# Performance work log

Hardware: AMD Instinct MI355X
Metric: run time of the kernel (lower is better)

## Reference

```python
import jax, jax.numpy as jnp
import numpy as np

N, D, H, L, T, R = 50000, 128, 8, 2, 4, 8
E = 800000
HD = D // H  # head_size = 16
SQRT_D = float(np.sqrt(HD))


def typed_linear(x, types, W):
    # x: (n, Din), types: (n,), W: (T, Din, Dout)  -- per-type dense projection
    out = jnp.zeros((x.shape[0], W.shape[-1]), x.dtype)
    for t in range(W.shape[0]):
        out = out + jnp.where((types == t)[:, None], x @ W[t], 0.0)
    return out


def rel_typed(x, etype, W):
    # x: (E, H, d), etype: (E,), W: (H, R, d, d) -- per-head, per-edge-type linear
    out = jnp.zeros_like(x)
    for r in range(W.shape[1]):
        out = out + jnp.where((etype == r)[:, None, None], jnp.einsum('ehd,hdo->eho', x, W[:, r]), 0.0)
    return out


def edge_softmax(a, dst, n):
    # softmax over incoming edges per destination node, per head. a: (E, H)
    amax = jax.ops.segment_max(a, dst, num_segments=n)
    amax = jnp.where(jnp.isfinite(amax), amax, 0.0)
    ex = jnp.exp(a - amax[dst])
    s = jax.ops.segment_sum(ex, dst, num_segments=n)
    return ex / (s[dst] + 1e-9)


def layer_norm(x, g, b, eps=1e-5):
    mu = x.mean(-1, keepdims=True)
    var = ((x - mu) ** 2).mean(-1, keepdims=True)
    return (x - mu) * jax.lax.rsqrt(var + eps) * g + b


def hgt_conv(x, ntype, etype, src, dst, Wk, Wq, Wv, Wa, ratt, rmsg, rpri, skip):
    n = x.shape[0]
    k = typed_linear(x, ntype, Wk).reshape(n, H, HD)
    q = typed_linear(x, ntype, Wq).reshape(n, H, HD)
    v = typed_linear(x, ntype, Wv).reshape(n, H, HD)
    kw = rel_typed(k[src], etype, ratt)               # (E, H, d)
    pri = rpri[:, etype].T                            # (E, H)
    a = (kw * q[dst]).sum(-1) * pri / SQRT_D          # (E, H)
    m = rel_typed(v[src], etype, rmsg)                # (E, H, d)
    att = edge_softmax(a, dst, n)                     # (E, H)
    h = jax.ops.segment_sum(m * att[..., None], dst, num_segments=n)
    h = h.reshape(n, D)
    h = typed_linear(h, ntype, Wa)                    # dropout off (eval)
    alpha = jax.nn.sigmoid(skip[ntype])[:, None]
    return h * alpha + x * (1.0 - alpha)


def setup_inputs() -> dict:
    key = jax.random.key(0)
    ks = jax.random.split(key, 12)
    g_lin = float(np.sqrt(2.0 / (D + D)))   # xavier-ish scale for D x D
    g_rel = float(np.sqrt(2.0 / (HD + HD)))
    g_emb = float(np.sqrt(2.0 / (N + D)))
    return {
        'embed': jax.random.normal(ks[0], (T, N, D), jnp.float32) * g_emb,
        'Wk': jax.random.normal(ks[1], (L, T, D, D), jnp.float32) * g_lin,
        'Wq': jax.random.normal(ks[2], (L, T, D, D), jnp.float32) * g_lin,
        'Wv': jax.random.normal(ks[3], (L, T, D, D), jnp.float32) * g_lin,
        'Wa': jax.random.normal(ks[4], (L, T, D, D), jnp.float32) * g_lin,
        'rel_att': jax.random.normal(ks[5], (L, H, R, HD, HD), jnp.float32) * g_rel,
        'rel_msg': jax.random.normal(ks[6], (L, H, R, HD, HD), jnp.float32) * g_rel,
        'rel_pri': jnp.ones((L, H, R), jnp.float32),
        'skip': jnp.ones((L, T), jnp.float32),
        'ln_g': jnp.ones((L, D), jnp.float32),
        'ln_b': jnp.zeros((L, D), jnp.float32),
        'src': jax.random.randint(ks[7], (E,), 0, N, jnp.int32),
        'dst': jax.random.randint(ks[8], (E,), 0, N, jnp.int32),
        'ntype': jax.random.randint(ks[9], (N,), 0, T, jnp.int32),
        'etype': jax.random.randint(ks[10], (E,), 0, R, jnp.int32),
    }


def reference(embed, Wk, Wq, Wv, Wa, rel_att, rel_msg, rel_pri, skip, ln_g, ln_b, src, dst, ntype, etype):
    # masked per-type embedding init: node gets row <rank-within-its-type> of its type table
    onehot = jax.nn.one_hot(ntype, T, dtype=jnp.int32)
    rank = jnp.take_along_axis(jnp.cumsum(onehot, axis=0), ntype[:, None], axis=1)[:, 0] - 1
    h = embed[ntype, rank]                            # (N, D)
    for l in range(L):
        h_prev = h
        hc = hgt_conv(h, ntype, etype, src, dst,
                      Wk[l], Wq[l], Wv[l], Wa[l],
                      rel_att[l], rel_msg[l], rel_pri[l], skip[l])
        h = layer_norm(hc, ln_g[l], ln_b[l]) + h_prev
    return h
```

## Files before the change

kernel.cpp:

```cpp
#include <hip/hip_runtime.h>
#include <math.h>

#define N_NODES 50000
#define DIM     128
#define NHEAD   8
#define HDIM    16
#define NLAYER  2
#define NTYPE   4
#define NREL    8
#define NEDGE   800000
#define RB      256
#define GN      8
#define MT      32
#define NK      (N_NODES * NREL)
#define LHR     (NLAYER * NHEAD * NREL)

typedef __attribute__((ext_vector_type(8))) short bf16x8;
typedef __attribute__((ext_vector_type(4))) float f32x4;

__device__ __forceinline__ float blo(unsigned w) { return __uint_as_float(w << 16); }
__device__ __forceinline__ float bhi(unsigned w) { return __uint_as_float(w & 0xFFFF0000u); }
__device__ __forceinline__ unsigned short f2bf(float f) {
    unsigned b = __float_as_uint(f);
    b += 0x7FFFu + ((b >> 16) & 1u);
    return (unsigned short)(b >> 16);
}
__device__ __forceinline__ bf16x8 pack8(float4 x0, float4 x1) {
    bf16x8 r;
    r[0] = (short)f2bf(x0.x); r[1] = (short)f2bf(x0.y);
    r[2] = (short)f2bf(x0.z); r[3] = (short)f2bf(x0.w);
    r[4] = (short)f2bf(x1.x); r[5] = (short)f2bf(x1.y);
    r[6] = (short)f2bf(x1.z); r[7] = (short)f2bf(x1.w);
    return r;
}
__device__ __forceinline__ bf16x8 zero8() {
    bf16x8 r;
    #pragma unroll
    for (int j = 0; j < 8; j++) r[j] = 0;
    return r;
}


__global__ void k_hist(const int* __restrict__ ntype, int* __restrict__ hist, int n) {
    __shared__ int cnt[NTYPE];
    if (threadIdx.x < NTYPE) cnt[threadIdx.x] = 0;
    __syncthreads();
    int i = blockIdx.x * RB + threadIdx.x;
    if (i < n) atomicAdd(&cnt[ntype[i]], 1);
    __syncthreads();
    if (threadIdx.x < NTYPE) hist[blockIdx.x * NTYPE + threadIdx.x] = cnt[threadIdx.x];
}

__global__ void k_prefix(const int* __restrict__ hist, int* __restrict__ off, int nb) {
    int t = threadIdx.x;
    if (t >= NTYPE) return;
    int acc = 0;
    for (int b = 0; b < nb; b++) { off[b * NTYPE + t] = acc; acc += hist[b * NTYPE + t]; }
}

__global__ void k_rank(const int* __restrict__ ntype, const int* __restrict__ off,
                       int* __restrict__ rank, int n) {
    __shared__ int ty[RB];
    int i = blockIdx.x * RB + threadIdx.x;
    int t = (i < n) ? ntype[i] : -1;
    ty[threadIdx.x] = t;
    __syncthreads();
    if (i < n) {
        int c = 0;
        for (int j = 0; j < (int)threadIdx.x; j++) c += (ty[j] == t);
        rank[i] = off[blockIdx.x * NTYPE + t] + c;
    }
}

__global__ void k_embed(const float* __restrict__ embed, const int* __restrict__ ntype,
                        const int* __restrict__ rank, float* __restrict__ h) {
    int i = blockIdx.x;
    int t = ntype[i], r = rank[i];
    h[(size_t)i * DIM + threadIdx.x] = embed[((size_t)t * N_NODES + r) * DIM + threadIdx.x];
}

__global__ void k_typeoff(const int* __restrict__ hist, const int* __restrict__ boff,
                          int nb, int* __restrict__ typeoff) {
    if (threadIdx.x == 0 && blockIdx.x == 0) {
        int acc = 0;
        for (int t = 0; t < NTYPE; t++) {
            typeoff[t] = acc;
            acc += boff[(nb - 1) * NTYPE + t] + hist[(nb - 1) * NTYPE + t];
        }
    }
}

__global__ void k_perm(const int* __restrict__ ntype, const int* __restrict__ rank,
                       const int* __restrict__ typeoff, int* __restrict__ perm,
                       int* __restrict__ iperm, int n) {
    int i = blockIdx.x * 256 + threadIdx.x;
    if (i < n) {
        int p = typeoff[ntype[i]] + rank[i];
        perm[p] = i;
        iperm[i] = p;
    }
}


__global__ void k_deg2(const int* __restrict__ dst, const int* __restrict__ etype,
                       int* __restrict__ deg) {
    int e = blockIdx.x * 256 + threadIdx.x;
    if (e < NEDGE) atomicAdd(&deg[dst[e] * NREL + etype[e]], 1);
}

__global__ void k_scan1(const int* __restrict__ deg, int* __restrict__ rs,
                        int* __restrict__ bsum, int n) {
    __shared__ int sh[256];
    int i = blockIdx.x * 256 + threadIdx.x;
    int v = (i < n) ? deg[i] : 0;
    sh[threadIdx.x] = v;
    __syncthreads();
    for (int off = 1; off < 256; off <<= 1) {
        int x = (threadIdx.x >= off) ? sh[threadIdx.x - off] : 0;
        __syncthreads();
        sh[threadIdx.x] += x;
        __syncthreads();
    }
    if (i < n) rs[i] = sh[threadIdx.x] - v;
    if (threadIdx.x == 255) bsum[blockIdx.x] = sh[255];
}

__global__ void k_scan2b(int* __restrict__ bsum, int nb) {
    __shared__ int sh[256];
    __shared__ int carry;
    if (threadIdx.x == 0) carry = 0;
    __syncthreads();
    for (int base = 0; base < nb; base += 256) {
        int i = base + threadIdx.x;
        int v = (i < nb) ? bsum[i] : 0;
        sh[threadIdx.x] = v;
        __syncthreads();
        for (int off = 1; off < 256; off <<= 1) {
            int x = (threadIdx.x >= off) ? sh[threadIdx.x - off] : 0;
            __syncthreads();
            sh[threadIdx.x] += x;
            __syncthreads();
        }
        if (i < nb) bsum[i] = sh[threadIdx.x] - v + carry;
        __syncthreads();
        if (threadIdx.x == 0) carry += sh[255];
        __syncthreads();
    }
}

__global__ void k_scan3(int* __restrict__ rs, const int* __restrict__ bsum, int n) {
    int i = blockIdx.x * 256 + threadIdx.x;
    if (i < n) rs[i] += bsum[blockIdx.x];
    if (i == 0) rs[n] = NEDGE;
}

__global__ void k_scatter2(const int* __restrict__ src, const int* __restrict__ dst,
                           const int* __restrict__ etype, const int* __restrict__ iperm,
                           const int* __restrict__ rs,
                           int* __restrict__ cur, int* __restrict__ epk) {
    int e = blockIdx.x * 256 + threadIdx.x;
    if (e < NEDGE) {
        int et = etype[e];
        int key = dst[e] * NREL + et;
        int p = atomicAdd(&cur[key], 1);
        epk[rs[key] + p] = iperm[src[e]] | (et << 24);
    }
}


__global__ void k_rattB(const float* __restrict__ ratt, unsigned short* __restrict__ rattB) {
    int i = blockIdx.x * 256 + threadIdx.x;
    rattB[i] = f2bf(ratt[i]);
}

__global__ void k_rmsgT(const float* __restrict__ rmsg, float* __restrict__ rmsgT) {
    int b = blockIdx.x;
    int d = threadIdx.x >> 4, o = threadIdx.x & 15;
    rmsgT[b * 256 + o * 16 + d] = rmsg[b * 256 + d * 16 + o];
}

__global__ void k_rmsgBP(const float* __restrict__ rmsg, unsigned short* __restrict__ out) {
    int b = blockIdx.x;
    int i = threadIdx.x;
    int ln = i >> 3, e = i & 7;
    int half = ln >> 4;
    unsigned short v = 0;
    if (half < 2) v = f2bf(rmsg[(size_t)b * 256 + (half * 8 + e) * 16 + (ln & 15)]);
    out[(size_t)b * 512 + i] = v;
}

__global__ void k_rattBP(const float* __restrict__ ratt, const float* __restrict__ rpri,
                         unsigned short* __restrict__ out) {
    int b = blockIdx.x;
    int i = threadIdx.x;
    int ln = i >> 3, e = i & 7;
    int half = ln >> 4;
    int et = b % NREL;
    int hh = (b / NREL) % NHEAD;
    int l = b / (NREL * NHEAD);
    float scale = rpri[(l * NHEAD + hh) * NREL + et] * 0.25f;
    unsigned short v = 0;
    if (half < 2) v = f2bf(ratt[(size_t)b * 256 + (half * 8 + e) * 16 + (ln & 15)] * scale);
    out[(size_t)b * 512 + i] = v;
}

__global__ void k_packW_all(const float* __restrict__ Wk, const float* __restrict__ Wq,
                            const float* __restrict__ Wv, unsigned short* __restrict__ wpk) {
    int bid = blockIdx.x;
    int t = bid & 3;
    int m = (bid >> 2) % 3;
    int l = bid / 12;
    const float* W = (m == 0 ? Wk : (m == 1 ? Wq : Wv)) + ((size_t)l * NTYPE + t) * 16384;
    unsigned short* ob = wpk + (size_t)bid * 16384;
    for (int idx = threadIdx.x; idx < 16384; idx += 256) {
        int ct = idx >> 11, kc = (idx >> 9) & 3, ln = (idx >> 3) & 63, j = idx & 7;
        int k = kc * 32 + ((ln >> 4) << 3) + j;
        int c = ct * 16 + (ln & 15);
        ob[idx] = f2bf(W[k * 128 + c]);
    }
}


template<int FULL>
__global__ __launch_bounds__(256) void k_qkv_mfma(
        const float* __restrict__ h, const int* __restrict__ perm, const int* __restrict__ ntype,
        const float* __restrict__ Wk, const float* __restrict__ Wq, const float* __restrict__ Wv,
        const unsigned short* __restrict__ WkB, const unsigned short* __restrict__ WqB,
        const unsigned short* __restrict__ WvB,
        const unsigned short* __restrict__ rattBP, const unsigned short* __restrict__ rmsgBP,
        const float* __restrict__ rmsgT,
        unsigned short* __restrict__ kb, float* __restrict__ qout,
        unsigned short* __restrict__ vt, unsigned short* __restrict__ tab, int n) {
    int tid = threadIdx.x;
    int base = blockIdx.x * MT;
    __shared__ int nodes_s[MT];
    __shared__ int types_s[MT];
    __shared__ unsigned short vs[MT][136];
    __shared__ unsigned short ks[MT][136];

    if (tid < MT) {
        int idx = base + tid;
        int nd = (idx < n) ? perm[idx] : -1;
        nodes_s[tid] = nd;
        types_s[tid] = (nd >= 0) ? ntype[nd] : -1;
    }
    __syncthreads();
    bool same = (nodes_s[MT - 1] >= 0) && (types_s[0] == types_s[MT - 1]);
    int l = tid & 63, w = tid >> 6;

    if (same) {
        int t = types_s[0];
        const unsigned short* wbk = WkB + (size_t)t * 16384;
        const unsigned short* wbq = WqB + (size_t)t * 16384;
        const unsigned short* wbv = WvB + (size_t)t * 16384;
        f32x4 acc[3][2][2];
        #pragma unroll
        for (int m = 0; m < 3; m++)
            #pragma unroll
            for (int a = 0; a < 2; a++)
                #pragma unroll
                for (int b = 0; b < 2; b++) {
                    acc[m][a][b][0] = 0.f; acc[m][a][b][1] = 0.f;
                    acc[m][a][b][2] = 0.f; acc[m][a][b][3] = 0.f;
                }
        #pragma unroll 1
        for (int kc = 0; kc < 4; kc++) {
            int koff = kc * 32 + ((l >> 4) << 3);
            int r0 = l & 15;
            const float4* p0 = (const float4*)(h + (size_t)nodes_s[r0] * DIM + koff);
            bf16x8 a0 = pack8(p0[0], p0[1]);
            const float4* p1 = (const float4*)(h + (size_t)nodes_s[16 + r0] * DIM + koff);
            bf16x8 a1 = pack8(p1[0], p1[1]);
            #pragma unroll
            for (int cti = 0; cti < 2; cti++) {
                int boff = ((w * 2 + cti) * 4 + kc) * 512 + l * 8;
                bf16x8 bk = *(const bf16x8*)(wbk + boff);
                acc[0][0][cti] = __builtin_amdgcn_mfma_f32_16x16x32_bf16(a0, bk, acc[0][0][cti], 0, 0, 0);
                acc[0][1][cti] = __builtin_amdgcn_mfma_f32_16x16x32_bf16(a1, bk, acc[0][1][cti], 0, 0, 0);
                bf16x8 bq = *(const bf16x8*)(wbq + boff);
                acc[1][0][cti] = __builtin_amdgcn_mfma_f32_16x16x32_bf16(a0, bq, acc[1][0][cti], 0, 0, 0);
                acc[1][1][cti] = __builtin_amdgcn_mfma_f32_16x16x32_bf16(a1, bq, acc[1][1][cti], 0, 0, 0);
                bf16x8 bv = *(const bf16x8*)(wbv + boff);
                acc[2][0][cti] = __builtin_amdgcn_mfma_f32_16x16x32_bf16(a0, bv, acc[2][0][cti], 0, 0, 0);
                acc[2][1][cti] = __builtin_amdgcn_mfma_f32_16x16x32_bf16(a1, bv, acc[2][1][cti], 0, 0, 0);
            }
        }
        #pragma unroll
        for (int mt = 0; mt < 2; mt++)
            #pragma unroll
            for (int cti = 0; cti < 2; cti++) {
                int col = w * 32 + cti * 16 + (l & 15);
                #pragma unroll
                for (int r = 0; r < 4; r++) {
                    int row = mt * 16 + ((l >> 4) << 2) + r;
                    size_t p = (size_t)(base + row) * DIM + col;
                    qout[p] = acc[1][mt][cti][r];
                    vs[row][col] = f2bf(acc[2][mt][cti][r]);
                    unsigned short kv = f2bf(acc[0][mt][cti][r]);
                    ks[row][col] = kv;
                    if constexpr (!FULL) kb[p] = kv;
                }
            }
    } else {
        int o = tid & 127, half = tid >> 7;
        for (int nn = half; nn < MT; nn += 2) {
            int nd = nodes_s[nn];
            if (nd < 0) { vs[nn][o] = 0; ks[nn][o] = 0; continue; }
            int t = types_s[nn];
            const float* wk = Wk + (size_t)t * 16384;
            const float* wq = Wq + (size_t)t * 16384;
            const float* wv = Wv + (size_t)t * 16384;
            float ak = 0.f, aq = 0.f, av = 0.f;
            for (int d = 0; d < DIM; d++) {
                float xv = h[(size_t)nd * DIM + d];
                ak = fmaf(xv, wk[d * DIM + o], ak);
                aq = fmaf(xv, wq[d * DIM + o], aq);
                av = fmaf(xv, wv[d * DIM + o], av);
            }
            size_t p = (size_t)(base + nn) * DIM + o;
            qout[p] = aq;
            vs[nn][o] = f2bf(av);
            unsigned short kv = f2bf(ak);
            ks[nn][o] = kv;
            if constexpr (!FULL) kb[p] = kv;
        }
    }
    __syncthreads();

    if constexpr (FULL) {
        __shared__ unsigned short tab_s[MT][264];
        int half = l >> 4;
        bf16x8 afrk[2][2], afrv[2][2];
        #pragma unroll
        for (int hh2 = 0; hh2 < 2; hh2++) {
            int hh = w * 2 + hh2;
            #pragma unroll
            for (int nt = 0; nt < 2; nt++) {
                if (half < 2) {
                    afrk[hh2][nt] = *(const bf16x8*)&ks[nt * 16 + (l & 15)][hh * HDIM + half * 8];
                    afrv[hh2][nt] = *(const bf16x8*)&vs[nt * 16 + (l & 15)][hh * HDIM + half * 8];
                } else {
                    afrk[hh2][nt] = zero8();
                    afrv[hh2][nt] = zero8();
                }
            }
        }
        #pragma unroll 1
        for (int et = 0; et < NREL; et++) {
            #pragma unroll
            for (int hh2 = 0; hh2 < 2; hh2++) {
                int hh = w * 2 + hh2;
                bf16x8 bfa = *(const bf16x8*)(rattBP + ((size_t)(hh * NREL + et) * 64 + l) * 8);
                bf16x8 bfm = *(const bf16x8*)(rmsgBP + ((size_t)(hh * NREL + et) * 64 + l) * 8);
                #pragma unroll
                for (int nt = 0; nt < 2; nt++) {
                    f32x4 dk = {0.f, 0.f, 0.f, 0.f};
                    dk = __builtin_amdgcn_mfma_f32_16x16x32_bf16(afrk[hh2][nt], bfa, dk, 0, 0, 0);
                    f32x4 dv = {0.f, 0.f, 0.f, 0.f};
                    dv = __builtin_amdgcn_mfma_f32_16x16x32_bf16(afrv[hh2][nt], bfm, dv, 0, 0, 0);
                    #pragma unroll
                    for (int r = 0; r < 4; r++) {
                        int row = nt * 16 + half * 4 + r;
                        tab_s[row][hh * HDIM + (l & 15)] = f2bf(dk[r]);
                        tab_s[row][128 + hh * HDIM + (l & 15)] = f2bf(dv[r]);
                    }
                }
            }
            __syncthreads();
            #pragma unroll
            for (int it = 0; it < 4; it++) {
                int idx = it * 256 + tid;
                int row = idx >> 5;
                int c8 = idx & 31;
                if (base + row < n)
                    *(uint4*)&tab[((size_t)(base + row) * NREL + et) * 256 + c8 * 8] =
                        *(const uint4*)&tab_s[row][c8 * 8];
            }
            __syncthreads();
        }
    } else {
        int o = tid & 127, half = tid >> 7;
        int hh = o >> 4, oo = o & 15;
        #pragma unroll 1
        for (int et = 0; et < NREL; et++) {
            const float4* wm4 = (const float4*)(rmsgT + ((size_t)(hh * NREL + et) * HDIM + oo) * HDIM);
            float4 m0 = wm4[0], m1 = wm4[1], m2 = wm4[2], m3 = wm4[3];
            for (int i = 0; i < 16; i++) {
                int nn = half * 16 + i;
                if (base + nn >= n) continue;
                const uint4* vr = (const uint4*)&vs[nn][hh * HDIM];
                uint4 v0 = vr[0], v1 = vr[1];
                float vv = blo(v0.x)*m0.x + bhi(v0.x)*m0.y + blo(v0.y)*m0.z + bhi(v0.y)*m0.w
                         + blo(v0.z)*m1.x + bhi(v0.z)*m1.y + blo(v0.w)*m1.z + bhi(v0.w)*m1.w
                         + blo(v1.x)*m2.x + bhi(v1.x)*m2.y + blo(v1.y)*m2.z + bhi(v1.y)*m2.w
                         + blo(v1.z)*m3.x + bhi(v1.z)*m3.y + blo(v1.w)*m3.z + bhi(v1.w)*m3.w;
                vt[((size_t)(base + nn) * NREL + et) * DIM + o] = f2bf(vv);
            }
        }
    }
}


__global__ __launch_bounds__(128) void k_fused12(
        const unsigned short* __restrict__ tab, const float* __restrict__ qbuf,
        const int* __restrict__ perm,
        const int* __restrict__ rs2, const int* __restrict__ epk,
        float* __restrict__ agg) {
    int b = blockIdx.x;
    int node = perm[b];
    int tid = threadIdx.x;
    int hh = tid >> 4, oo = tid & 15;
    int wv = tid >> 6;
    int hl = hh & 3;

    __shared__ float q_s[DIM];
    __shared__ float a_sw[2][4][HDIM + 1];
    __shared__ int   es_sw[2][HDIM];

    int e0 = rs2[node * NREL];
    int e1 = rs2[node * NREL + NREL];
    if (e0 == e1) { agg[(size_t)b * DIM + tid] = 0.f; return; }

    q_s[tid] = qbuf[(size_t)b * DIM + tid];
    const float4* q4 = (const float4*)&q_s[hh * HDIM];
    float4 q0 = q4[0], q1 = q4[1], q2 = q4[2], q3 = q4[3];

    float m_h = -1e30f, s_h = 0.f, out = 0.f;

    for (int w0e = e0; w0e < e1; w0e += HDIM) {
        int cnt = min(HDIM, e1 - w0e);
        float a = -1e30f;
        int pk = 0;
        if (oo < cnt) {
            pk = epk[w0e + oo];
            int sv = pk & 0x00FFFFFF;
            int et = ((unsigned)pk) >> 24;
            const uint4* kw = (const uint4*)(tab + ((size_t)sv * NREL + et) * 256 + hh * HDIM);
            uint4 ka = kw[0], kc = kw[1];
            a = blo(ka.x)*q0.x + bhi(ka.x)*q0.y + blo(ka.y)*q0.z + bhi(ka.y)*q0.w
              + blo(ka.z)*q1.x + bhi(ka.z)*q1.y + blo(ka.w)*q1.z + bhi(ka.w)*q1.w
              + blo(kc.x)*q2.x + bhi(kc.x)*q2.y + blo(kc.y)*q2.z + bhi(kc.y)*q2.w
              + blo(kc.z)*q3.x + bhi(kc.z)*q3.y + blo(kc.w)*q3.z + bhi(kc.w)*q3.w;
        }
        if (hl == 0) es_sw[wv][oo] = pk;
        float cmax = a;
        cmax = fmaxf(cmax, __shfl_xor(cmax, 1));
        cmax = fmaxf(cmax, __shfl_xor(cmax, 2));
        cmax = fmaxf(cmax, __shfl_xor(cmax, 4));
        cmax = fmaxf(cmax, __shfl_xor(cmax, 8));
        float m_t = (cmax > m_h + 12.f) ? cmax : m_h;
        float r = __expf(m_h - m_t);
        s_h *= r; out *= r; m_h = m_t;
        float p = (oo < cnt) ? __expf(a - m_h) : 0.f;
        float ps = p;
        ps += __shfl_xor(ps, 1);
        ps += __shfl_xor(ps, 2);
        ps += __shfl_xor(ps, 4);
        ps += __shfl_xor(ps, 8);
        s_h += ps;
        a_sw[wv][hl][oo] = p;
        for (int c = 0; c < cnt; c++) {
            float pc = a_sw[wv][hl][c];
            int pkc = es_sw[wv][c];
            int sv = pkc & 0x00FFFFFF;
            int et = ((unsigned)pkc) >> 24;
            unsigned short uv = tab[((size_t)sv * NREL + et) * 256 + 128 + tid];
            out = fmaf(pc, __uint_as_float((unsigned)uv << 16), out);
        }
    }

    agg[(size_t)b * DIM + tid] = out / (s_h + 1e-9f);
}


__global__ __launch_bounds__(128) void k_fused11(
        const unsigned short* __restrict__ kb, const float* __restrict__ qbuf,
        const unsigned short* __restrict__ vt,
        const int* __restrict__ perm,
        const int* __restrict__ rs2, const int* __restrict__ epk,
        const unsigned short* __restrict__ rattB, const float* __restrict__ rpri,
        float* __restrict__ agg) {
    int b = blockIdx.x;
    int node = perm[b];
    int tid = threadIdx.x;
    int hh = tid >> 4, oo = tid & 15;
    int wv = tid >> 6;
    int hl = hh & 3;

    __shared__ float q_s[DIM];
    __shared__ float u_s[NREL][NHEAD * HDIM + 4];
    __shared__ float a_sw[2][4][HDIM + 1];
    __shared__ int   es_sw[2][HDIM];

    int e0 = rs2[node * NREL];
    int e1 = rs2[node * NREL + NREL];
    if (e0 == e1) { agg[(size_t)b * DIM + tid] = 0.f; return; }

    q_s[tid] = qbuf[(size_t)b * DIM + tid];
    {
        const float4* q4 = (const float4*)&q_s[hh * HDIM];
        float4 q0 = q4[0], q1 = q4[1], q2 = q4[2], q3 = q4[3];
        #pragma unroll
        for (int et = 0; et < NREL; et++) {
            const uint4* wB = (const uint4*)(rattB + ((size_t)(hh * NREL + et) * HDIM + oo) * HDIM);
            uint4 wa = wB[0], wb = wB[1];
            float s = blo(wa.x)*q0.x + bhi(wa.x)*q0.y + blo(wa.y)*q0.z + bhi(wa.y)*q0.w
                    + blo(wa.z)*q1.x + bhi(wa.z)*q1.y + blo(wa.w)*q1.z + bhi(wa.w)*q1.w
                    + blo(wb.x)*q2.x + bhi(wb.x)*q2.y + blo(wb.y)*q2.z + bhi(wb.y)*q2.w
                    + blo(wb.z)*q3.x + bhi(wb.z)*q3.y + blo(wb.w)*q3.z + bhi(wb.w)*q3.w;
            u_s[et][tid] = s * rpri[hh * NREL + et] * 0.25f;
        }
    }

    float m_h = -1e30f, s_h = 0.f, out = 0.f;

    for (int w0e = e0; w0e < e1; w0e += HDIM) {
        int cnt = min(HDIM, e1 - w0e);
        float a = -1e30f;
        int pk = 0;
        if (oo < cnt) {
            pk = epk[w0e + oo];
            int sv = pk & 0x00FFFFFF;
            int et = ((unsigned)pk) >> 24;
            const uint4* kr = (const uint4*)(kb + (size_t)sv * DIM + hh * HDIM);
            uint4 ka = kr[0], kc = kr[1];
            const float4* u4 = (const float4*)&u_s[et][hh * HDIM];
            float4 u0 = u4[0], u1 = u4[1], u2 = u4[2], u3 = u4[3];
            a = blo(ka.x)*u0.x + bhi(ka.x)*u0.y + blo(ka.y)*u0.z + bhi(ka.y)*u0.w
              + blo(ka.z)*u1.x + bhi(ka.z)*u1.y + blo(ka.w)*u1.z + bhi(ka.w)*u1.w
              + blo(kc.x)*u2.x + bhi(kc.x)*u2.y + blo(kc.y)*u2.z + bhi(kc.y)*u2.w
              + blo(kc.z)*u3.x + bhi(kc.z)*u3.y + blo(kc.w)*u3.z + bhi(kc.w)*u3.w;
        }
        if (hl == 0) es_sw[wv][oo] = pk;
        float cmax = a;
        cmax = fmaxf(cmax, __shfl_xor(cmax, 1));
        cmax = fmaxf(cmax, __shfl_xor(cmax, 2));
        cmax = fmaxf(cmax, __shfl_xor(cmax, 4));
        cmax = fmaxf(cmax, __shfl_xor(cmax, 8));
        float m_t = (cmax > m_h + 12.f) ? cmax : m_h;
        float r = __expf(m_h - m_t);
        s_h *= r; out *= r; m_h = m_t;
        float p = (oo < cnt) ? __expf(a - m_h) : 0.f;
        float ps = p;
        ps += __shfl_xor(ps, 1);
        ps += __shfl_xor(ps, 2);
        ps += __shfl_xor(ps, 4);
        ps += __shfl_xor(ps, 8);
        s_h += ps;
        a_sw[wv][hl][oo] = p;
        for (int c = 0; c < cnt; c++) {
            float pc = a_sw[wv][hl][c];
            int pkc = es_sw[wv][c];
            int sv = pkc & 0x00FFFFFF;
            int et = ((unsigned)pkc) >> 24;
            unsigned short uv = vt[((size_t)sv * NREL + et) * DIM + tid];
            out = fmaf(pc, __uint_as_float((unsigned)uv << 16), out);
        }
    }

    agg[(size_t)b * DIM + tid] = out / (s_h + 1e-9f);
}


__global__ __launch_bounds__(128) void k_out_g(
        const float* __restrict__ agg, float* __restrict__ h,
        const int* __restrict__ perm, const int* __restrict__ ntype,
        const float* __restrict__ Wa, const float* __restrict__ skip,
        const float* __restrict__ ln_g, const float* __restrict__ ln_b, int n) {
    int o = threadIdx.x;
    int base = blockIdx.x * GN;
    __shared__ float xs[GN][DIM];
    __shared__ float hcs[GN][DIM + 1];
    __shared__ int nodes[GN];
    __shared__ int types[GN];
    __shared__ float mu_s[GN], rs_s[GN];
    if (o < GN) {
        int idx = base + o;
        int nd = (idx < n) ? perm[idx] : -1;
        nodes[o] = nd;
        types[o] = (nd >= 0) ? ntype[nd] : -1;
    }
    __syncthreads();
    #pragma unroll
    for (int nn = 0; nn < GN; nn++)
        if (nodes[nn] >= 0) xs[nn][o] = agg[(size_t)(base + nn) * DIM + o];
    __syncthreads();
    bool same = (nodes[GN - 1] >= 0) && (types[0] == types[GN - 1]);
    if (same) {
        int t = types[0];
        const float* w = Wa + (size_t)t * DIM * DIM;
        float acc[GN];
        #pragma unroll
        for (int nn = 0; nn < GN; nn++) acc[nn] = 0.f;
        for (int d = 0; d < DIM; d++) {
            float wv = w[d * DIM + o];
            #pragma unroll
            for (int nn = 0; nn < GN; nn++) acc[nn] = fmaf(xs[nn][d], wv, acc[nn]);
        }
        float alpha = 1.f / (1.f + __expf(-skip[t]));
        #pragma unroll
        for (int nn = 0; nn < GN; nn++) {
            float hp = h[(size_t)nodes[nn] * DIM + o];
            hcs[nn][o] = acc[nn] * alpha + hp * (1.f - alpha);
        }
    } else {
        #pragma unroll 1
        for (int nn = 0; nn < GN; nn++) {
            if (nodes[nn] < 0) continue;
            int t = types[nn];
            const float* w = Wa + (size_t)t * DIM * DIM;
            float a0 = 0.f;
            for (int d = 0; d < DIM; d++) a0 = fmaf(xs[nn][d], w[d * DIM + o], a0);
            float alpha = 1.f / (1.f + __expf(-skip[t]));
            float hp = h[(size_t)nodes[nn] * DIM + o];
            hcs[nn][o] = a0 * alpha + hp * (1.f - alpha);
        }
    }
    __syncthreads();
    {
        int g = o >> 4, j = o & 15;
        if (nodes[g] >= 0) {
            float s = 0.f;
            for (int d = j; d < DIM; d += 16) s += hcs[g][d];
            #pragma unroll
            for (int m = 1; m < 16; m <<= 1) s += __shfl_xor(s, m);
            float mu = s * (1.f / DIM);
            float v = 0.f;
            for (int d = j; d < DIM; d += 16) { float dv = hcs[g][d] - mu; v = fmaf(dv, dv, v); }
            #pragma unroll
            for (int m = 1; m < 16; m <<= 1) v += __shfl_xor(v, m);
            if (j == 0) { mu_s[g] = mu; rs_s[g] = rsqrtf(v * (1.f / DIM) + 1e-5f); }
        }
    }
    __syncthreads();
    float g_o = ln_g[o], b_o = ln_b[o];
    #pragma unroll
    for (int nn = 0; nn < GN; nn++) {
        if (nodes[nn] >= 0) {
            float hp = h[(size_t)nodes[nn] * DIM + o];
            h[(size_t)nodes[nn] * DIM + o] = (hcs[nn][o] - mu_s[nn]) * rs_s[nn] * g_o + b_o + hp;
        }
    }
}


extern "C" void kernel_launch(void* const* d_in, const int* in_sizes, int n_in,
                              void* d_out, int out_size, void* d_ws, size_t ws_size,
                              hipStream_t stream) {
    const float* embed = (const float*)d_in[0];
    const float* Wk    = (const float*)d_in[1];
    const float* Wq    = (const float*)d_in[2];
    const float* Wv    = (const float*)d_in[3];
    const float* Wa    = (const float*)d_in[4];
    const float* ratt  = (const float*)d_in[5];
    const float* rmsg  = (const float*)d_in[6];
    const float* rpri  = (const float*)d_in[7];
    const float* skip  = (const float*)d_in[8];
    const float* ln_g  = (const float*)d_in[9];
    const float* ln_b  = (const float*)d_in[10];
    const int*   src   = (const int*)d_in[11];
    const int*   dst   = (const int*)d_in[12];
    const int*   ntype = (const int*)d_in[13];
    const int*   etype = (const int*)d_in[14];

    float* h = (float*)d_out;

    const size_t ND = (size_t)N_NODES * DIM;
    const int nb = (N_NODES + RB - 1) / RB;
    unsigned short* kb = (unsigned short*)d_ws;
    float* qbuf = (float*)(kb + ND);
    int* rs2  = (int*)(qbuf + ND);
    int* deg2 = rs2 + (NK + 1);
    int* cur2 = deg2 + NK;
    int* epk  = cur2 + NK;
    int* bsum = epk + NEDGE;
    int* rank = bsum + 2048;
    int* hist = rank + N_NODES;
    int* boff = hist + nb * NTYPE;
    int* typeoff = boff + nb * NTYPE;
    int* perm = typeoff + NTYPE;
    int* iperm = perm + N_NODES;
    float* rmsgT = (float*)(iperm + N_NODES);
    unsigned short* rattB  = (unsigned short*)(rmsgT + (size_t)LHR * 256);
    unsigned short* rattBP = rattB + (size_t)LHR * 256;
    unsigned short* rmsgBP = rattBP + (size_t)LHR * 512;
    unsigned short* wpk = rmsgBP + (size_t)LHR * 512;
    unsigned short* vt  = wpk + (size_t)NLAYER * 3 * NTYPE * 16384;
    unsigned short* tab = vt;
    size_t need_full = (size_t)((char*)(tab + (size_t)N_NODES * NREL * 256) - (char*)d_ws);
    const bool FULL = (ws_size >= need_full);
    float* agg = qbuf;

    const int EB = (NEDGE + 255) / 256;
    const int nb2 = (NK + 255) / 256;

    k_hist<<<nb, RB, 0, stream>>>(ntype, hist, N_NODES);
    k_prefix<<<1, 64, 0, stream>>>(hist, boff, nb);
    k_rank<<<nb, RB, 0, stream>>>(ntype, boff, rank, N_NODES);
    k_embed<<<N_NODES, DIM, 0, stream>>>(embed, ntype, rank, h);
    k_typeoff<<<1, 64, 0, stream>>>(hist, boff, nb, typeoff);
    k_perm<<<nb, 256, 0, stream>>>(ntype, rank, typeoff, perm, iperm, N_NODES);

    hipMemsetAsync(deg2, 0, (size_t)NK * sizeof(int), stream);
    hipMemsetAsync(cur2, 0, (size_t)NK * sizeof(int), stream);
    k_deg2<<<EB, 256, 0, stream>>>(dst, etype, deg2);
    k_scan1<<<nb2, 256, 0, stream>>>(deg2, rs2, bsum, NK);
    k_scan2b<<<1, 256, 0, stream>>>(bsum, nb2);
    k_scan3<<<nb2, 256, 0, stream>>>(rs2, bsum, NK);
    k_scatter2<<<EB, 256, 0, stream>>>(src, dst, etype, iperm, rs2, cur2, epk);

    k_rmsgT<<<LHR, 256, 0, stream>>>(rmsg, rmsgT);
    k_rattB<<<LHR, 256, 0, stream>>>(ratt, rattB);
    k_rattBP<<<LHR, 512, 0, stream>>>(ratt, rpri, rattBP);
    k_rmsgBP<<<LHR, 512, 0, stream>>>(rmsg, rmsgBP);
    k_packW_all<<<NLAYER * 3 * NTYPE, 256, 0, stream>>>(Wk, Wq, Wv, wpk);

    const int NGB = N_NODES / GN;
    const int NMB = (N_NODES + MT - 1) / MT;

    for (int l = 0; l < NLAYER; l++) {
        const float* Wk_l = Wk + (size_t)l * NTYPE * DIM * DIM;
        const float* Wq_l = Wq + (size_t)l * NTYPE * DIM * DIM;
        const float* Wv_l = Wv + (size_t)l * NTYPE * DIM * DIM;
        const float* Wa_l = Wa + (size_t)l * NTYPE * DIM * DIM;
        const unsigned short* wkB_l = wpk + ((size_t)l * 3 + 0) * NTYPE * 16384;
        const unsigned short* wqB_l = wpk + ((size_t)l * 3 + 1) * NTYPE * 16384;
        const unsigned short* wvB_l = wpk + ((size_t)l * 3 + 2) * NTYPE * 16384;
        const unsigned short* rattB_l  = rattB + (size_t)l * NHEAD * NREL * 256;
        const unsigned short* rattBP_l = rattBP + (size_t)l * NHEAD * NREL * 512;
        const unsigned short* rmsgBP_l = rmsgBP + (size_t)l * NHEAD * NREL * 512;
        const float* rmsgT_l = rmsgT + (size_t)l * NHEAD * NREL * 256;
        const float* rpri_l = rpri + (size_t)l * NHEAD * NREL;
        const float* skip_l = skip + (size_t)l * NTYPE;
        const float* g_l = ln_g + (size_t)l * DIM;
        const float* b_l = ln_b + (size_t)l * DIM;

        if (FULL) {
            k_qkv_mfma<1><<<NMB, 256, 0, stream>>>(h, perm, ntype, Wk_l, Wq_l, Wv_l,
                                                   wkB_l, wqB_l, wvB_l,
                                                   rattBP_l, rmsgBP_l, rmsgT_l,
                                                   kb, qbuf, vt, tab, N_NODES);
            k_fused12<<<N_NODES, 128, 0, stream>>>(tab, qbuf, perm, rs2, epk, agg);
        } else {
            k_qkv_mfma<0><<<NMB, 256, 0, stream>>>(h, perm, ntype, Wk_l, Wq_l, Wv_l,
                                                   wkB_l, wqB_l, wvB_l,
                                                   rattBP_l, rmsgBP_l, rmsgT_l,
                                                   kb, qbuf, vt, tab, N_NODES);
            k_fused11<<<N_NODES, 128, 0, stream>>>(kb, qbuf, vt, perm, rs2, epk,
                                                   rattB_l, rpri_l, agg);
        }
        k_out_g<<<NGB, 128, 0, stream>>>(agg, h, perm, ntype, Wa_l, skip_l, g_l, b_l, N_NODES);
    }
}
```

Measured before the change: 722.0 us.

## Use bf16 MFMA for output projection and merge shared buffers in QKV kernel

Replaces the scalar fp32 output-projection/layernorm kernel with an MFMA version that processes 32 type-sorted nodes per block using pre-packed bf16 Wa weights. The packing kernel now also packs Wa, and the workspace layout changes to match. The QKV kernel merges its k/v and table shared-memory arrays into one pool to cut LDS use, which needs an extra barrier. Converting agg to bf16 lowers precision of the output projection.

```diff
diff --git a/kernel.cpp b/kernel.cpp
--- a/kernel.cpp
+++ b/kernel.cpp
@@ -10,7 +10,6 @@
 #define NREL    8
 #define NEDGE   800000
 #define RB      256
-#define GN      8
 #define MT      32
 #define NK      (N_NODES * NREL)
 #define LHR     (NLAYER * NHEAD * NREL)
@@ -205,12 +204,14 @@
 }
 
 __global__ void k_packW_all(const float* __restrict__ Wk, const float* __restrict__ Wq,
-                            const float* __restrict__ Wv, unsigned short* __restrict__ wpk) {
+                            const float* __restrict__ Wv, const float* __restrict__ Wa,
+                            unsigned short* __restrict__ wpk) {
     int bid = blockIdx.x;
     int t = bid & 3;
-    int m = (bid >> 2) % 3;
-    int l = bid / 12;
-    const float* W = (m == 0 ? Wk : (m == 1 ? Wq : Wv)) + ((size_t)l * NTYPE + t) * 16384;
+    int m = (bid >> 2) & 3;
+    int l = bid >> 4;
+    const float* W = (m == 0 ? Wk : (m == 1 ? Wq : (m == 2 ? Wv : Wa)))
+                     + ((size_t)l * NTYPE + t) * 16384;
     unsigned short* ob = wpk + (size_t)bid * 16384;
     for (int idx = threadIdx.x; idx < 16384; idx += 256) {
         int ct = idx >> 11, kc = (idx >> 9) & 3, ln = (idx >> 3) & 63, j = idx & 7;
@@ -235,8 +236,7 @@
     int base = blockIdx.x * MT;
     __shared__ int nodes_s[MT];
     __shared__ int types_s[MT];
-    __shared__ unsigned short vs[MT][136];
-    __shared__ unsigned short ks[MT][136];
+    __shared__ unsigned short pool[MT][272];
 
     if (tid < MT) {
         int idx = base + tid;
@@ -295,9 +295,9 @@
                     int row = mt * 16 + ((l >> 4) << 2) + r;
                     size_t p = (size_t)(base + row) * DIM + col;
                     qout[p] = acc[1][mt][cti][r];
-                    vs[row][col] = f2bf(acc[2][mt][cti][r]);
+                    pool[row][136 + col] = f2bf(acc[2][mt][cti][r]);
                     unsigned short kv = f2bf(acc[0][mt][cti][r]);
-                    ks[row][col] = kv;
+                    pool[row][col] = kv;
                     if constexpr (!FULL) kb[p] = kv;
                 }
             }
@@ -305,7 +305,7 @@
         int o = tid & 127, half = tid >> 7;
         for (int nn = half; nn < MT; nn += 2) {
             int nd = nodes_s[nn];
-            if (nd < 0) { vs[nn][o] = 0; ks[nn][o] = 0; continue; }
+            if (nd < 0) { pool[nn][136 + o] = 0; pool[nn][o] = 0; continue; }
             int t = types_s[nn];
             const float* wk = Wk + (size_t)t * 16384;
             const float* wq = Wq + (size_t)t * 16384;
@@ -319,16 +319,15 @@
             }
             size_t p = (size_t)(base + nn) * DIM + o;
             qout[p] = aq;
-            vs[nn][o] = f2bf(av);
+            pool[nn][136 + o] = f2bf(av);
             unsigned short kv = f2bf(ak);
-            ks[nn][o] = kv;
+            pool[nn][o] = kv;
             if constexpr (!FULL) kb[p] = kv;
         }
     }
     __syncthreads();
 
     if constexpr (FULL) {
-        __shared__ unsigned short tab_s[MT][264];
         int half = l >> 4;
         bf16x8 afrk[2][2], afrv[2][2];
         #pragma unroll
@@ -337,14 +336,15 @@
             #pragma unroll
             for (int nt = 0; nt < 2; nt++) {
                 if (half < 2) {
-                    afrk[hh2][nt] = *(const bf16x8*)&ks[nt * 16 + (l & 15)][hh * HDIM + half * 8];
-                    afrv[hh2][nt] = *(const bf16x8*)&vs[nt * 16 + (l & 15)][hh * HDIM + half * 8];
+                    afrk[hh2][nt] = *(const bf16x8*)&pool[nt * 16 + (l & 15)][hh * HDIM + half * 8];
+                    afrv[hh2][nt] = *(const bf16x8*)&pool[nt * 16 + (l & 15)][136 + hh * HDIM + half * 8];
                 } else {
                     afrk[hh2][nt] = zero8();
                     afrv[hh2][nt] = zero8();
                 }
             }
         }
+        __syncthreads();
         #pragma unroll 1
         for (int et = 0; et < NREL; et++) {
             #pragma unroll
@@ -361,8 +361,8 @@
                     #pragma unroll
                     for (int r = 0; r < 4; r++) {
                         int row = nt * 16 + half * 4 + r;
-                        tab_s[row][hh * HDIM + (l & 15)] = f2bf(dk[r]);
-                        tab_s[row][128 + hh * HDIM + (l & 15)] = f2bf(dv[r]);
+                        pool[row][hh * HDIM + (l & 15)] = f2bf(dk[r]);
+                        pool[row][128 + hh * HDIM + (l & 15)] = f2bf(dv[r]);
                     }
                 }
             }
@@ -374,7 +374,7 @@
                 int c8 = idx & 31;
                 if (base + row < n)
                     *(uint4*)&tab[((size_t)(base + row) * NREL + et) * 256 + c8 * 8] =
-                        *(const uint4*)&tab_s[row][c8 * 8];
+                        *(const uint4*)&pool[row][c8 * 8];
             }
             __syncthreads();
         }
@@ -388,7 +388,7 @@
             for (int i = 0; i < 16; i++) {
                 int nn = half * 16 + i;
                 if (base + nn >= n) continue;
-                const uint4* vr = (const uint4*)&vs[nn][hh * HDIM];
+                const uint4* vr = (const uint4*)&pool[nn][136 + hh * HDIM];
                 uint4 v0 = vr[0], v1 = vr[1];
                 float vv = blo(v0.x)*m0.x + bhi(v0.x)*m0.y + blo(v0.y)*m0.z + bhi(v0.y)*m0.w
                          + blo(v0.z)*m1.x + bhi(v0.z)*m1.y + blo(v0.w)*m1.z + bhi(v0.w)*m1.w
@@ -562,83 +562,114 @@
 }
 
 
-__global__ __launch_bounds__(128) void k_out_g(
+__global__ __launch_bounds__(256) void k_out_mfma(
         const float* __restrict__ agg, float* __restrict__ h,
         const int* __restrict__ perm, const int* __restrict__ ntype,
-        const float* __restrict__ Wa, const float* __restrict__ skip,
+        const float* __restrict__ Wa, const unsigned short* __restrict__ WaB,
+        const float* __restrict__ skip,
         const float* __restrict__ ln_g, const float* __restrict__ ln_b, int n) {
-    int o = threadIdx.x;
-    int base = blockIdx.x * GN;
-    __shared__ float xs[GN][DIM];
-    __shared__ float hcs[GN][DIM + 1];
-    __shared__ int nodes[GN];
-    __shared__ int types[GN];
-    __shared__ float mu_s[GN], rs_s[GN];
-    if (o < GN) {
-        int idx = base + o;
+    int tid = threadIdx.x;
+    int base = blockIdx.x * MT;
+    __shared__ int nodes_s[MT];
+    __shared__ int types_s[MT];
+    __shared__ float hc[MT][132];
+    __shared__ float mu_s[MT], rsg[MT];
+
+    if (tid < MT) {
+        int idx = base + tid;
         int nd = (idx < n) ? perm[idx] : -1;
-        nodes[o] = nd;
-        types[o] = (nd >= 0) ? ntype[nd] : -1;
-    }
-    __syncthreads();
-    #pragma unroll
-    for (int nn = 0; nn < GN; nn++)
-        if (nodes[nn] >= 0) xs[nn][o] = agg[(size_t)(base + nn) * DIM + o];
-    __syncthreads();
-    bool same = (nodes[GN - 1] >= 0) && (types[0] == types[GN - 1]);
+        nodes_s[tid] = nd;
+        types_s[tid] = (nd >= 0) ? ntype[nd] : -1;
+    }
+    __syncthreads();
+    bool same = (nodes_s[MT - 1] >= 0) && (types_s[0] == types_s[MT - 1]);
+    int l = tid & 63, w = tid >> 6;
+
     if (same) {
-        int t = types[0];
-        const float* w = Wa + (size_t)t * DIM * DIM;
-        float acc[GN];
+        int t = types_s[0];
+        const unsigned short* wb = WaB + (size_t)t * 16384;
+        f32x4 acc[2][2];
         #pragma unroll
-        for (int nn = 0; nn < GN; nn++) acc[nn] = 0.f;
-        for (int d = 0; d < DIM; d++) {
-            float wv = w[d * DIM + o];
-            #pragma unroll
-            for (int nn = 0; nn < GN; nn++) acc[nn] = fmaf(xs[nn][d], wv, acc[nn]);
+        for (int a = 0; a < 2; a++)
+            #pragma unroll
+            for (int b = 0; b < 2; b++) {
+                acc[a][b][0] = 0.f; acc[a][b][1] = 0.f;
+                acc[a][b][2] = 0.f; acc[a][b][3] = 0.f;
+            }
+        #pragma unroll 1
+        for (int kc = 0; kc < 4; kc++) {
+            int koff = kc * 32 + ((l >> 4) << 3);
+            int r0 = l & 15;
+            const float4* p0 = (const float4*)(agg + (size_t)(base + r0) * DIM + koff);
+            bf16x8 a0 = pack8(p0[0], p0[1]);
+            const float4* p1 = (const float4*)(agg + (size_t)(base + 16 + r0) * DIM + koff);
+            bf16x8 a1 = pack8(p1[0], p1[1]);
+            #pragma unroll
+            for (int cti = 0; cti < 2; cti++) {
+                int boff = ((w * 2 + cti) * 4 + kc) * 512 + l * 8;
+                bf16x8 bw = *(const bf16x8*)(wb + boff);
+                acc[0][cti] = __builtin_amdgcn_mfma_f32_16x16x32_bf16(a0, bw, acc[0][cti], 0, 0, 0);
+                acc[1][cti] = __builtin_amdgcn_mfma_f32_16x16x32_bf16(a1, bw, acc[1][cti], 0, 0, 0);
+            }
         }
         float alpha = 1.f / (1.f + __expf(-skip[t]));
         #pragma unroll
-        for (int nn = 0; nn < GN; nn++) {
-            float hp = h[(size_t)nodes[nn] * DIM + o];
-            hcs[nn][o] = acc[nn] * alpha + hp * (1.f - alpha);
-        }
+        for (int mt = 0; mt < 2; mt++)
+            #pragma unroll
+            for (int cti = 0; cti < 2; cti++) {
+                int col = w * 32 + cti * 16 + (l & 15);
+                #pragma unroll
+                for (int r = 0; r < 4; r++) {
+                    int row = mt * 16 + ((l >> 4) << 2) + r;
+                    float hp = h[(size_t)nodes_s[row] * DIM + col];
+                    hc[row][col] = acc[mt][cti][r] * alpha + hp * (1.f - alpha);
+                }
+            }
     } else {
-        #pragma unroll 1
-        for (int nn = 0; nn < GN; nn++) {
-            if (nodes[nn] < 0) continue;
-            int t = types[nn];
-            const float* w = Wa + (size_t)t * DIM * DIM;
+        int o = tid & 127, half = tid >> 7;
+        for (int nn = half; nn < MT; nn += 2) {
+            int nd = nodes_s[nn];
+            if (nd < 0) continue;
+            int t = types_s[nn];
+            const float* wv = Wa + (size_t)t * 16384;
             float a0 = 0.f;
-            for (int d = 0; d < DIM; d++) a0 = fmaf(xs[nn][d], w[d * DIM + o], a0);
+            for (int d = 0; d < DIM; d++)
+                a0 = fmaf(agg[(size_t)(base + nn) * DIM + d], wv[d * DIM + o], a0);
             float alpha = 1.f / (1.f + __expf(-skip[t]));
-            float hp = h[(size_t)nodes[nn] * DIM + o];
-            hcs[nn][o] = a0 * alpha + hp * (1.f - alpha);
+            float hp = h[(size_t)nd * DIM + o];
+            hc[nn][o] = a0 * alpha + hp * (1.f - alpha);
         }
     }
     __syncthreads();
     {
-        int g = o >> 4, j = o & 15;
-        if (nodes[g] >= 0) {
+        int row = tid >> 3, j = tid & 7;
+        if (nodes_s[row] >= 0) {
             float s = 0.f;
-            for (int d = j; d < DIM; d += 16) s += hcs[g][d];
-            #pragma unroll
-            for (int m = 1; m < 16; m <<= 1) s += __shfl_xor(s, m);
+            for (int d = j; d < DIM; d += 8) s += hc[row][d];
+            s += __shfl_xor(s, 1);
+            s += __shfl_xor(s, 2);
+            s += __shfl_xor(s, 4);
             float mu = s * (1.f / DIM);
             float v = 0.f;
-            for (int d = j; d < DIM; d += 16) { float dv = hcs[g][d] - mu; v = fmaf(dv, dv, v); }
-            #pragma unroll
-            for (int m = 1; m < 16; m <<= 1) v += __shfl_xor(v, m);
-            if (j == 0) { mu_s[g] = mu; rs_s[g] = rsqrtf(v * (1.f / DIM) + 1e-5f); }
-        }
-    }
-    __syncthreads();
-    float g_o = ln_g[o], b_o = ln_b[o];
-    #pragma unroll
-    for (int nn = 0; nn < GN; nn++) {
-        if (nodes[nn] >= 0) {
-            float hp = h[(size_t)nodes[nn] * DIM + o];
-            h[(size_t)nodes[nn] * DIM + o] = (hcs[nn][o] - mu_s[nn]) * rs_s[nn] * g_o + b_o + hp;
+            for (int d = j; d < DIM; d += 8) { float dv = hc[row][d] - mu; v = fmaf(dv, dv, v); }
+            v += __shfl_xor(v, 1);
+            v += __shfl_xor(v, 2);
+            v += __shfl_xor(v, 4);
+            if (j == 0) { mu_s[row] = mu; rsg[row] = rsqrtf(v * (1.f / DIM) + 1e-5f); }
+        }
+    }
+    __syncthreads();
+    {
+        int row = tid >> 3, j = tid & 7;
+        int nd = nodes_s[row];
+        if (nd >= 0) {
+            float mu = mu_s[row], rs = rsg[row];
+            #pragma unroll
+            for (int c = 0; c < 16; c++) {
+                int col = j * 16 + c;
+                float hp = h[(size_t)nd * DIM + col];
+                h[(size_t)nd * DIM + col] = (hc[row][col] - mu) * rs * ln_g[col] + ln_b[col] + hp;
+            }
         }
     }
 }
@@ -685,7 +716,7 @@
     unsigned short* rattBP = rattB + (size_t)LHR * 256;
     unsigned short* rmsgBP = rattBP + (size_t)LHR * 512;
     unsigned short* wpk = rmsgBP + (size_t)LHR * 512;
-    unsigned short* vt  = wpk + (size_t)NLAYER * 3 * NTYPE * 16384;
+    unsigned short* vt  = wpk + (size_t)NLAYER * 4 * NTYPE * 16384;
     unsigned short* tab = vt;
     size_t need_full = (size_t)((char*)(tab + (size_t)N_NODES * NREL * 256) - (char*)d_ws);
     const bool FULL = (ws_size >= need_full);
@@ -713,9 +744,8 @@
     k_rattB<<<LHR, 256, 0, stream>>>(ratt, rattB);
     k_rattBP<<<LHR, 512, 0, stream>>>(ratt, rpri, rattBP);
     k_rmsgBP<<<LHR, 512, 0, stream>>>(rmsg, rmsgBP);
-    k_packW_all<<<NLAYER * 3 * NTYPE, 256, 0, stream>>>(Wk, Wq, Wv, wpk);
-
-    const int NGB = N_NODES / GN;
+    k_packW_all<<<NLAYER * 4 * NTYPE, 256, 0, stream>>>(Wk, Wq, Wv, Wa, wpk);
+
     const int NMB = (N_NODES + MT - 1) / MT;
 
     for (int l = 0; l < NLAYER; l++) {
@@ -723,9 +753,10 @@
         const float* Wq_l = Wq + (size_t)l * NTYPE * DIM * DIM;
         const float* Wv_l = Wv + (size_t)l * NTYPE * DIM * DIM;
         const float* Wa_l = Wa + (size_t)l * NTYPE * DIM * DIM;
-        const unsigned short* wkB_l = wpk + ((size_t)l * 3 + 0) * NTYPE * 16384;
-        const unsigned short* wqB_l = wpk + ((size_t)l * 3 + 1) * NTYPE * 16384;
-        const unsigned short* wvB_l = wpk + ((size_t)l * 3 + 2) * NTYPE * 16384;
+        const unsigned short* wkB_l = wpk + ((size_t)l * 4 + 0) * NTYPE * 16384;
+        const unsigned short* wqB_l = wpk + ((size_t)l * 4 + 1) * NTYPE * 16384;
+        const unsigned short* wvB_l = wpk + ((size_t)l * 4 + 2) * NTYPE * 16384;
+        const unsigned short* waB_l = wpk + ((size_t)l * 4 + 3) * NTYPE * 16384;
         const unsigned short* rattB_l  = rattB + (size_t)l * NHEAD * NREL * 256;
         const unsigned short* rattBP_l = rattBP + (size_t)l * NHEAD * NREL * 512;
         const unsigned short* rmsgBP_l = rmsgBP + (size_t)l * NHEAD * NREL * 512;
@@ -749,6 +780,7 @@
             k_fused11<<<N_NODES, 128, 0, stream>>>(kb, qbuf, vt, perm, rs2, epk,
                                                    rattB_l, rpri_l, agg);
         }
-        k_out_g<<<NGB, 128, 0, stream>>>(agg, h, perm, ntype, Wa_l, skip_l, g_l, b_l, N_NODES);
-    }
-}
+        k_out_mfma<<<NMB, 256, 0, stream>>>(agg, h, perm, ntype, Wa_l, waB_l,
+                                            skip_l, g_l, b_l, N_NODES);
+    }
+}
```

Measured after the change: 726.7 us. About the same (+0.7%).
